# Performance work log

Measured on AMD Instinct MI355X. Metric: run time of the kernel, lower is better.

Reference implementation:

```python
import jax, jax.numpy as jnp
import numpy as np

RC = 5.2                                   # radial cutoff Rcr
ETA_R = np.array([16.0], dtype=np.float32)
SHF_R = (0.9 + 0.26875 * np.arange(16)).astype(np.float32)
NUM_SPECIES = 4                             # len(vocabulary)


def setup_inputs() -> dict:
    key = jax.random.key(0)
    kp, ks = jax.random.split(key)
    B, N = 64, 256
    # random positions in a 12 A box -> realistic distance matrices
    pos = jax.random.uniform(kp, (B, N, 3), jnp.float32, 0.0, 12.0)
    diff = pos[:, :, None, :] - pos[:, None, :, :]
    d = jnp.sqrt(jnp.sum(diff * diff, axis=-1) + 1e-12)
    d = d * (1.0 - jnp.eye(N, dtype=jnp.float32))  # zero self-distance
    species = jax.random.randint(ks, (B, N), 1, NUM_SPECIES + 1, jnp.int32)
    return {"distance_matrices_batch": d, "num_species_batch": species}


def reference(distance_matrices_batch, num_species_batch):
    d = distance_matrices_batch                      # [B, N, N]
    eta = jnp.asarray(ETA_R)
    shf = jnp.asarray(SHF_R)
    # cartesian product of (EtaR, ShfR), P = len(EtaR)*len(ShfR)
    eta_p = jnp.repeat(eta, shf.shape[0])            # [P]
    shf_p = jnp.tile(shf, eta.shape[0])              # [P]

    mask = (d < RC) & (d != 0.0)                     # [B, N, N]
    fc = 0.5 * jnp.cos(jnp.pi * d / RC) + 0.5        # ANAKIN cutoff fn
    # Gaussian radial terms, masked to the cutoff neighborhood
    terms = jnp.exp(-eta_p * (d[..., None] - shf_p) ** 2) * fc[..., None]  # [B,N,N,P]
    terms = jnp.where(mask[..., None], terms, jnp.zeros((), terms.dtype))

    # one-hot of neighbor species (IDs are 1-based)
    oh = jax.nn.one_hot(num_species_batch - 1, NUM_SPECIES, dtype=terms.dtype)  # [B,N,S]
    # scatter-sum over neighbors j, bucketed by species of j
    GR = jnp.einsum('bijp,bjs->bisp', terms, oh)     # [B, N, S, P]
    B, N = d.shape[0], d.shape[1]
    return GR.reshape(B, N, NUM_SPECIES * terms.shape[-1])  # [B, N, S*P]
```

## Files before the change

### kernel.cpp

```cpp
#include <hip/hip_runtime.h>
#include <stdint.h>


static __device__ __forceinline__ int mbcnt64(uint64_t m) {
    int lo = __builtin_amdgcn_mbcnt_lo((uint32_t)m, 0u);
    return __builtin_amdgcn_mbcnt_hi((uint32_t)(m >> 32), lo);
}

__global__ __launch_bounds__(256) void aev_kernel(
    const float* __restrict__ dmat,
    const int* __restrict__ species,
    float* __restrict__ out)
{
    __shared__ alignas(16) float2 comp[8][288];
    __shared__ alignas(16) int pos[256];
    __shared__ int cntm[4][4];

    const int tid  = threadIdx.x;
    const int w    = tid >> 6;
    const int lane = tid & 63;
    const int blk  = (int)blockIdx.x;
    const int row0 = blk * 8 + w * 2;
    const int b    = blk >> 5;

    const float4 qa = ((const float4*)(dmat + ((size_t)row0 << 8)))[lane];
    const float4 qb = ((const float4*)(dmat + ((size_t)(row0 + 1) << 8)))[lane];

    int sj = species[(b << 8) + tid] - 1;
    sj = (sj < 0) ? 0 : ((sj > 3) ? 3 : sj);
    const uint64_t bs0 = __ballot((sj & 1) != 0);
    const uint64_t bs1 = __ballot((sj & 2) != 0);
    const uint64_t m0 = ~bs0 & ~bs1, m1 = bs0 & ~bs1;
    const uint64_t m2 = ~bs0 &  bs1, m3 = bs0 &  bs1;
    if (lane == 0) {
        cntm[w][0] = __popcll(m0); cntm[w][1] = __popcll(m1);
        cntm[w][2] = __popcll(m2); cntm[w][3] = __popcll(m3);
    }
    uint64_t msel = m0;
    msel = (sj == 1) ? m1 : msel;
    msel = (sj == 2) ? m2 : msel;
    msel = (sj == 3) ? m3 : msel;
    const int rank = mbcnt64(msel);

    {
        float2* cz = &comp[0][0];
        #pragma unroll
        for (int k = 0; k < 9; ++k) cz[tid + 256 * k] = make_float2(2.6f, 0.0f);
    }
    __syncthreads();

    int segP[5], nIt[4];
    segP[0] = 0;
    #pragma unroll
    for (int s = 0; s < 4; ++s) {
        const int t4  = cntm[0][s] + cntm[1][s] + cntm[2][s] + cntm[3][s];
        const int t4p = (t4 + 7) & ~7;
        nIt[s]     = t4p >> 3;
        segP[s + 1] = segP[s] + t4p;
    }
    {
        int base = segP[0];
        base = (sj == 1) ? segP[1] : base;
        base = (sj == 2) ? segP[2] : base;
        base = (sj == 3) ? segP[3] : base;
        int wadd = 0;
        #pragma unroll
        for (int w2 = 0; w2 < 3; ++w2) wadd += (w2 < w) ? cntm[w2][sj] : 0;
        const int slot = base + wadd + rank;
        pos[tid] = (slot < 287) ? slot : 287;
    }
    __syncthreads();

    {
        const int4 p4 = *(const int4*)&pos[4 * lane];
        const int   pp[4] = {p4.x, p4.y, p4.z, p4.w};
        const float da[4] = {qa.x, qa.y, qa.z, qa.w};
        const float db[4] = {qb.x, qb.y, qb.z, qb.w};
        const int lr = w * 2;
        #pragma unroll
        for (int e = 0; e < 4; ++e) {
            const float dd = da[e];
            const bool  v  = (dd < 5.2f) && (dd != 0.0f);
            const float x  = v ? dd : 2.6f;
            const float fc = 0.5f * __builtin_amdgcn_cosf(x * (0.5f / 5.2f)) + 0.5f;
            comp[lr][pp[e]] = make_float2(x, v ? fc : 0.0f);
        }
        #pragma unroll
        for (int e = 0; e < 4; ++e) {
            const float dd = db[e];
            const bool  v  = (dd < 5.2f) && (dd != 0.0f);
            const float x  = v ? dd : 2.6f;
            const float fc = 0.5f * __builtin_amdgcn_cosf(x * (0.5f / 5.2f)) + 0.5f;
            comp[lr + 1][pp[e]] = make_float2(x, v ? fc : 0.0f);
        }
    }
    __syncthreads();

    const int p = lane >> 2;
    const int q = lane & 3;
    const float shfp = 0.9f + 0.26875f * (float)p;
    const int lr = w * 2;
    float acc[2][4];
    #pragma unroll
    for (int s = 0; s < 4; ++s) {
        float a0 = 0.0f, a1 = 0.0f;
        const int k0 = segP[s] + 2 * q;
        const int n  = nIt[s];
        for (int m = 0; m < n; ++m) {
            const int k = k0 + 8 * m;
            const float4 f0 = *(const float4*)&comp[lr][k];
            const float4 f1 = *(const float4*)&comp[lr + 1][k];
            float u;
            u = f0.x - shfp; a0 = __builtin_fmaf(__builtin_amdgcn_exp2f(u * u * -23.083120654223414f), f0.y, a0);
            u = f0.z - shfp; a0 = __builtin_fmaf(__builtin_amdgcn_exp2f(u * u * -23.083120654223414f), f0.w, a0);
            u = f1.x - shfp; a1 = __builtin_fmaf(__builtin_amdgcn_exp2f(u * u * -23.083120654223414f), f1.y, a1);
            u = f1.z - shfp; a1 = __builtin_fmaf(__builtin_amdgcn_exp2f(u * u * -23.083120654223414f), f1.w, a1);
        }
        acc[0][s] = a0; acc[1][s] = a1;
    }
    #pragma unroll
    for (int rr = 0; rr < 2; ++rr)
        #pragma unroll
        for (int s = 0; s < 4; ++s) {
            acc[rr][s] += __shfl_xor(acc[rr][s], 1, 64);
            acc[rr][s] += __shfl_xor(acc[rr][s], 2, 64);
        }
    #pragma unroll
    for (int rr = 0; rr < 2; ++rr) {
        float vout = acc[rr][0];
        vout = (q == 1) ? acc[rr][1] : vout;
        vout = (q == 2) ? acc[rr][2] : vout;
        vout = (q == 3) ? acc[rr][3] : vout;
        __builtin_nontemporal_store(vout,
            &out[((size_t)(row0 + rr) << 6) + (size_t)((q << 4) + p)]);
    }
}

extern "C" void kernel_launch(void* const* d_in, const int* in_sizes, int n_in,
                              void* d_out, int out_size, void* d_ws, size_t ws_size,
                              hipStream_t stream) {
    const float* dmat  = (const float*)d_in[0];
    const int* species = (const int*)d_in[1];
    float* o           = (float*)d_out;
    const int B = in_sizes[1] >> 8;
    aev_kernel<<<dim3(B * 32), 256, 0, stream>>>(dmat, species, o);
}
```

Measured before the change: 79.66 us.

## Fold cutoff and Gaussian into single exp2 via log-space precompute; remap lanes

Each neighbor entry now stores log2(fc) - K*d^2 and a linear coefficient, so every Gaussian term becomes one FMA, one add and one exp2, with no separate multiply by fc. Lanes are remapped so each thread handles four shifts and one species segment, reusing each loaded entry across four exponentials. Segments are no longer padded to multiples of 8, which removes the shared-memory zero-fill. Results are reduced through shuffles and a small LDS buffer, then written as vectorized stores. The risks are log-domain precision loss, extra iterations on the longest species segment, and an added LDS round trip without a barrier (each wave reads only its own rows).

```diff
diff --git a/kernel.cpp b/kernel.cpp
--- a/kernel.cpp
+++ b/kernel.cpp
@@ -7,13 +7,18 @@
     return __builtin_amdgcn_mbcnt_hi((uint32_t)(m >> 32), lo);
 }
 
+typedef float vfloat2 __attribute__((ext_vector_type(2)));
+
+#define KNEG (-23.083120654223414f)
+
 __global__ __launch_bounds__(256) void aev_kernel(
     const float* __restrict__ dmat,
     const int* __restrict__ species,
     float* __restrict__ out)
 {
-    __shared__ alignas(16) float2 comp[8][288];
-    __shared__ alignas(16) int pos[256];
+    __shared__ alignas(16) float2 comp[8][256];
+    __shared__ alignas(16) int    pos[256];
+    __shared__ alignas(16) float  red[8][64];
     __shared__ int cntm[4][4];
 
     const int tid  = threadIdx.x;
@@ -41,33 +46,22 @@
     msel = (sj == 2) ? m2 : msel;
     msel = (sj == 3) ? m3 : msel;
     const int rank = mbcnt64(msel);
-
-    {
-        float2* cz = &comp[0][0];
-        #pragma unroll
-        for (int k = 0; k < 9; ++k) cz[tid + 256 * k] = make_float2(2.6f, 0.0f);
-    }
     __syncthreads();
 
-    int segP[5], nIt[4];
-    segP[0] = 0;
+    int seg[5];
+    seg[0] = 0;
     #pragma unroll
-    for (int s = 0; s < 4; ++s) {
-        const int t4  = cntm[0][s] + cntm[1][s] + cntm[2][s] + cntm[3][s];
-        const int t4p = (t4 + 7) & ~7;
-        nIt[s]     = t4p >> 3;
-        segP[s + 1] = segP[s] + t4p;
-    }
+    for (int s = 0; s < 4; ++s)
+        seg[s + 1] = seg[s] + cntm[0][s] + cntm[1][s] + cntm[2][s] + cntm[3][s];
     {
-        int base = segP[0];
-        base = (sj == 1) ? segP[1] : base;
-        base = (sj == 2) ? segP[2] : base;
-        base = (sj == 3) ? segP[3] : base;
+        int base = seg[0];
+        base = (sj == 1) ? seg[1] : base;
+        base = (sj == 2) ? seg[2] : base;
+        base = (sj == 3) ? seg[3] : base;
         int wadd = 0;
         #pragma unroll
         for (int w2 = 0; w2 < 3; ++w2) wadd += (w2 < w) ? cntm[w2][sj] : 0;
-        const int slot = base + wadd + rank;
-        pos[tid] = (slot < 287) ? slot : 287;
+        pos[tid] = base + wadd + rank;
     }
     __syncthreads();
 
@@ -76,6 +70,7 @@
         const int   pp[4] = {p4.x, p4.y, p4.z, p4.w};
         const float da[4] = {qa.x, qa.y, qa.z, qa.w};
         const float db[4] = {qb.x, qb.y, qb.z, qb.w};
+        const float NINF = -__builtin_inff();
         const int lr = w * 2;
         #pragma unroll
         for (int e = 0; e < 4; ++e) {
@@ -83,7 +78,8 @@
             const bool  v  = (dd < 5.2f) && (dd != 0.0f);
             const float x  = v ? dd : 2.6f;
             const float fc = 0.5f * __builtin_amdgcn_cosf(x * (0.5f / 5.2f)) + 0.5f;
-            comp[lr][pp[e]] = make_float2(x, v ? fc : 0.0f);
+            const float cA = __builtin_fmaf(KNEG * x, x, __builtin_amdgcn_logf(fc));
+            comp[lr][pp[e]] = make_float2(v ? cA : NINF, v ? (-2.0f * KNEG) * x : 0.0f);
         }
         #pragma unroll
         for (int e = 0; e < 4; ++e) {
@@ -91,48 +87,76 @@
             const bool  v  = (dd < 5.2f) && (dd != 0.0f);
             const float x  = v ? dd : 2.6f;
             const float fc = 0.5f * __builtin_amdgcn_cosf(x * (0.5f / 5.2f)) + 0.5f;
-            comp[lr + 1][pp[e]] = make_float2(x, v ? fc : 0.0f);
+            const float cA = __builtin_fmaf(KNEG * x, x, __builtin_amdgcn_logf(fc));
+            comp[lr + 1][pp[e]] = make_float2(v ? cA : NINF, v ? (-2.0f * KNEG) * x : 0.0f);
         }
     }
     __syncthreads();
 
-    const int p = lane >> 2;
-    const int q = lane & 3;
-    const float shfp = 0.9f + 0.26875f * (float)p;
+    const int g  = lane >> 4;
+    const int qp = (lane >> 2) & 3;
+    const int sp = lane & 3;
     const int lr = w * 2;
-    float acc[2][4];
+
+    float shf[4], kp[4];
     #pragma unroll
-    for (int s = 0; s < 4; ++s) {
-        float a0 = 0.0f, a1 = 0.0f;
-        const int k0 = segP[s] + 2 * q;
-        const int n  = nIt[s];
-        for (int m = 0; m < n; ++m) {
-            const int k = k0 + 8 * m;
-            const float4 f0 = *(const float4*)&comp[lr][k];
-            const float4 f1 = *(const float4*)&comp[lr + 1][k];
-            float u;
-            u = f0.x - shfp; a0 = __builtin_fmaf(__builtin_amdgcn_exp2f(u * u * -23.083120654223414f), f0.y, a0);
-            u = f0.z - shfp; a0 = __builtin_fmaf(__builtin_amdgcn_exp2f(u * u * -23.083120654223414f), f0.w, a0);
-            u = f1.x - shfp; a1 = __builtin_fmaf(__builtin_amdgcn_exp2f(u * u * -23.083120654223414f), f1.y, a1);
-            u = f1.z - shfp; a1 = __builtin_fmaf(__builtin_amdgcn_exp2f(u * u * -23.083120654223414f), f1.w, a1);
+    for (int t = 0; t < 4; ++t) {
+        shf[t] = 0.9f + 0.26875f * (float)(4 * g + t);
+        kp[t]  = KNEG * shf[t] * shf[t];
+    }
+
+    const int sbeg = (sp == 0) ? seg[0] : (sp == 1) ? seg[1] : (sp == 2) ? seg[2] : seg[3];
+    const int send = (sp == 0) ? seg[1] : (sp == 1) ? seg[2] : (sp == 2) ? seg[3] : seg[4];
+    int maxLen = seg[1] - seg[0];
+    maxLen = (seg[2] - seg[1] > maxLen) ? seg[2] - seg[1] : maxLen;
+    maxLen = (seg[3] - seg[2] > maxLen) ? seg[3] - seg[2] : maxLen;
+    maxLen = (seg[4] - seg[3] > maxLen) ? seg[4] - seg[3] : maxLen;
+    const int nIt = (maxLen + 3) >> 2;
+
+    const float NINF = -__builtin_inff();
+    float a0x = 0.f, a0y = 0.f, a0z = 0.f, a0w = 0.f;
+    float a1x = 0.f, a1y = 0.f, a1z = 0.f, a1w = 0.f;
+    for (int m = 0; m < nIt; ++m) {
+        const int k  = sbeg + qp + 4 * m;
+        const int kc = (k < 255) ? k : 255;
+        const bool live = (k < send);
+        const float2 cR0 = comp[lr][kc];
+        const float2 cR1 = comp[lr + 1][kc];
+        const float A0 = live ? cR0.x : NINF;
+        const float A1 = live ? cR1.x : NINF;
+        #pragma unroll
+        for (int t = 0; t < 4; ++t) {
+            const float e0 = __builtin_amdgcn_exp2f(__builtin_fmaf(cR0.y, shf[t], A0) + kp[t]);
+            const float e1 = __builtin_amdgcn_exp2f(__builtin_fmaf(cR1.y, shf[t], A1) + kp[t]);
+            if (t == 0) { a0x += e0; a1x += e1; }
+            if (t == 1) { a0y += e0; a1y += e1; }
+            if (t == 2) { a0z += e0; a1z += e1; }
+            if (t == 3) { a0w += e0; a1w += e1; }
         }
-        acc[0][s] = a0; acc[1][s] = a1;
     }
+
     #pragma unroll
-    for (int rr = 0; rr < 2; ++rr)
-        #pragma unroll
-        for (int s = 0; s < 4; ++s) {
-            acc[rr][s] += __shfl_xor(acc[rr][s], 1, 64);
-            acc[rr][s] += __shfl_xor(acc[rr][s], 2, 64);
-        }
-    #pragma unroll
-    for (int rr = 0; rr < 2; ++rr) {
-        float vout = acc[rr][0];
-        vout = (q == 1) ? acc[rr][1] : vout;
-        vout = (q == 2) ? acc[rr][2] : vout;
-        vout = (q == 3) ? acc[rr][3] : vout;
-        __builtin_nontemporal_store(vout,
-            &out[((size_t)(row0 + rr) << 6) + (size_t)((q << 4) + p)]);
+    for (int d = 4; d <= 8; d <<= 1) {
+        a0x += __shfl_xor(a0x, d, 64); a0y += __shfl_xor(a0y, d, 64);
+        a0z += __shfl_xor(a0z, d, 64); a0w += __shfl_xor(a0w, d, 64);
+        a1x += __shfl_xor(a1x, d, 64); a1y += __shfl_xor(a1y, d, 64);
+        a1z += __shfl_xor(a1z, d, 64); a1w += __shfl_xor(a1w, d, 64);
+    }
+
+    if (qp == 0) {
+        float4* r0 = (float4*)&red[lr][(sp << 4) + (g << 2)];
+        float4* r1 = (float4*)&red[lr + 1][(sp << 4) + (g << 2)];
+        *r0 = make_float4(a0x, a0y, a0z, a0w);
+        *r1 = make_float4(a1x, a1y, a1z, a1w);
+    }
+
+    {
+        const int r  = lane >> 5;
+        const int c2 = lane & 31;
+        const float2 rv = ((const float2*)&red[lr + r][0])[c2];
+        vfloat2 nv; nv.x = rv.x; nv.y = rv.y;
+        vfloat2* dst = (vfloat2*)&out[((size_t)(row0 + r) << 6) + (size_t)(c2 * 2)];
+        __builtin_nontemporal_store(nv, dst);
     }
 }
 
```

Result: faster. 75.83 us (-4.8%).
